# Kernel tuning notes

Hardware: AMD Instinct MI355X
Metric: run time of the kernel (lower is better)

The kernel has to match this reference:

```python
import jax, jax.numpy as jnp
import numpy as np

B, N, H, NB, NCT = 8, 4096, 1024, 128, 33
LN_EPS = 1e-5


def setup_inputs() -> dict:
    key = jax.random.key(0)
    ks = jax.random.split(key, 12)
    x = jax.random.normal(ks[0], (B, N, H), dtype=jnp.float32)
    cancer_type = jax.random.randint(ks[1], (B,), 0, NCT)
    block_ids = jax.random.randint(ks[2], (B, N), 0, NB)
    pad_mask = jnp.zeros((B, N), dtype=bool)
    s1 = 1.0 / np.sqrt(H)
    s2 = 1.0 / np.sqrt(H // 2)
    return {
        "x": x,
        "cancer_type": cancer_type,
        "block_ids": block_ids,
        "pad_mask": pad_mask,
        "W1": jax.random.normal(ks[3], (H, H // 2), jnp.float32) * s1,
        "b1": jnp.zeros((H // 2,), jnp.float32),
        "W2": jax.random.normal(ks[4], (H // 2, 1), jnp.float32) * s2,
        "b2": jnp.zeros((1,), jnp.float32),
        "ct_emb": jax.random.normal(ks[5], (NCT, NB), jnp.float32) * 0.1,
        "Wp": jax.random.normal(ks[6], (H, H), jnp.float32) * s1,
        "bp": jnp.zeros((H,), jnp.float32),
        "ln_g": jnp.ones((H,), jnp.float32),
        "ln_b": jnp.zeros((H,), jnp.float32),
    }


def reference(x, cancer_type, block_ids, pad_mask, W1, b1, W2, b2, ct_emb, Wp, bp, ln_g, ln_b):
    nb = ct_emb.shape[1]
    # gate MLP: (B,N)
    h = jnp.tanh(x @ W1 + b1)
    gate = (h @ W2 + b2)[..., 0]
    valid = ~pad_mask
    # block membership mask (B, NB, N)
    mask = (block_ids[:, None, :] == jnp.arange(nb)[None, :, None]) & valid[:, None, :]
    neg_inf = jnp.float32(-jnp.inf)
    scores = jnp.where(mask, gate[:, None, :], neg_inf)
    # stable masked softmax over N; empty blocks -> all-zero weights (nan_to_num(0))
    m = jnp.max(scores, axis=-1, keepdims=True)
    m = jnp.where(jnp.isfinite(m), m, 0.0)
    e = jnp.where(mask, jnp.exp(scores - m), 0.0)
    denom = jnp.sum(e, axis=-1, keepdims=True)
    w = jnp.where(denom > 0, e / jnp.maximum(denom, 1e-30), 0.0)
    # cancer-type modulation: weights * (1 + 0.1*ct_mod[:,bid])
    ct_mod = ct_emb[cancer_type]  # (B, NB)
    w = w * (1.0 + 0.1 * ct_mod)[:, :, None]
    # pooled per-block token (B, NB, H)
    pooled = jnp.einsum('bkn,bnh->bkh', w, x)
    # block_proj: Linear -> LayerNorm -> ELU (dropout = eval identity)
    y = pooled @ Wp + bp
    mu = jnp.mean(y, axis=-1, keepdims=True)
    var = jnp.mean((y - mu) ** 2, axis=-1, keepdims=True)
    y = (y - mu) * jax.lax.rsqrt(var + LN_EPS) * ln_g + ln_b
    y = jax.nn.elu(y)
    has_b = jnp.any(mask, axis=-1)              # (B, NB)
    present = jnp.any(has_b, axis=0)            # (NB,) torch loop skips blocks absent everywhere
    block_tokens = jnp.where(present[None, :, None], y, 0.0)
    return block_tokens, has_b
```

## Files before the change

kernel.cpp:

```cpp
#include <hip/hip_runtime.h>

#define NTOK 4096
#define HDIM 1024
#define HHALF 512
#define NBLK 128
#define CAP 256

typedef __attribute__((ext_vector_type(8))) short short8;
typedef __attribute__((ext_vector_type(4))) float f32x4;
typedef short bf16s;

__device__ __forceinline__ short f2bf(float f) {
    unsigned u = __builtin_bit_cast(unsigned, f);
    u = (u + 0x7fffu + ((u >> 16) & 1u)) >> 16;
    return (short)u;
}
__device__ __forceinline__ void gload_lds16(const void* g, void* l) {
    __builtin_amdgcn_global_load_lds(
        (const __attribute__((address_space(1))) unsigned int*)g,
        (__attribute__((address_space(3))) unsigned int*)l, 16, 0, 0);
}
__device__ __forceinline__ float fast_tanh(float v) {
    float e = __expf(2.0f * v);
    return 1.0f - 2.0f / (e + 1.0f);
}

__global__ void k_tcvt2(const float* __restrict__ W1, const float* __restrict__ Wp,
                        bf16s* __restrict__ w1t, bf16s* __restrict__ wpt) {
    __shared__ float tile[64][65];
    const int by = blockIdx.y;
    const float* in = (by < 8) ? W1 : Wp;
    bf16s* out = (by < 8) ? w1t : wpt;
    const int Nc = (by < 8) ? HHALF : HDIM;
    const int n0 = ((by < 8) ? by : (by - 8)) * 64;
    const int k0 = blockIdx.x * 64;
    const int tx = threadIdx.x & 63, ty = threadIdx.x >> 6;
    #pragma unroll
    for (int i = 0; i < 16; ++i) {
        int r = ty + i * 4;
        tile[r][tx] = in[(size_t)(k0 + r) * Nc + n0 + tx];
    }
    __syncthreads();
    #pragma unroll
    for (int i = 0; i < 16; ++i) {
        int r = ty + i * 4;
        out[(size_t)(n0 + r) * 1024 + k0 + tx] = f2bf(tile[tx][r]);
    }
}

__global__ __launch_bounds__(256, 3) void k_gemm_gf(
    const float* __restrict__ x, const bf16s* __restrict__ w1t,
    const float* __restrict__ b1, const float* __restrict__ w2,
    float* __restrict__ partial)
{
    __shared__ alignas(16) float As[2][128 * 32];
    __shared__ alignas(16) bf16s Bs[2][128 * 32];
    __shared__ float gp[2][128];

    const int tid = threadIdx.x;
    const int lane = tid & 63;
    const int wv = tid >> 6;
    const int wr = wv >> 1, wc = wv & 1;
    const int phys = blockIdx.x;
    const int logical = (phys & 7) * 128 + (phys >> 3);
    const int row0 = (logical >> 2) * 128;
    const int col0 = (logical & 3) * 128;
    const int c0 = lane & 15, khalf = lane >> 4;

    const int aRow = wv * 32 + (lane >> 3);
    const int aj = (lane & 7) ^ ((lane >> 3) & 7);
    const float* aSrc = &x[(size_t)(row0 + aRow) * HDIM + aj * 4];
    const int adst = wv * 1024 + lane * 4;

    const int bRow = wv * 32 + (lane >> 2);
    const int bj = (lane & 3) ^ ((lane >> 3) & 3);
    const bf16s* bSrc = &w1t[(size_t)(col0 + bRow) * HDIM + bj * 8];
    const int bdst = wv * 1024 + lane * 8;

    f32x4 acc[4][4] = {};

    #pragma unroll
    for (int q = 0; q < 4; ++q)
        gload_lds16(aSrc + q * 8 * HDIM, &As[0][adst + q * 256]);
    #pragma unroll
    for (int q = 0; q < 2; ++q)
        gload_lds16(bSrc + q * 16 * HDIM, &Bs[0][bdst + q * 512]);

    for (int t = 0; t < 32; ++t) {
        const int cur = t & 1;
        if (t < 31) {
            const int ko = (t + 1) * 32;
            #pragma unroll
            for (int q = 0; q < 4; ++q)
                gload_lds16(aSrc + q * 8 * HDIM + ko, &As[cur ^ 1][adst + q * 256]);
            #pragma unroll
            for (int q = 0; q < 2; ++q)
                gload_lds16(bSrc + q * 16 * HDIM + ko, &Bs[cur ^ 1][bdst + q * 512]);
            asm volatile("s_waitcnt vmcnt(6)" ::: "memory");
        } else {
            asm volatile("s_waitcnt vmcnt(0)" ::: "memory");
        }
        __builtin_amdgcn_s_barrier();
        __builtin_amdgcn_sched_barrier(0);

        short8 av[4], bv[4];
        #pragma unroll
        for (int mf = 0; mf < 4; ++mf) {
            int ra = wr * 64 + mf * 16 + c0;
            f32x4 lo = *reinterpret_cast<const f32x4*>(
                &As[cur][ra * 32 + (((2 * khalf) ^ (ra & 7)) * 4)]);
            f32x4 hi = *reinterpret_cast<const f32x4*>(
                &As[cur][ra * 32 + (((2 * khalf + 1) ^ (ra & 7)) * 4)]);
            short h[8] = {f2bf(lo[0]), f2bf(lo[1]), f2bf(lo[2]), f2bf(lo[3]),
                          f2bf(hi[0]), f2bf(hi[1]), f2bf(hi[2]), f2bf(hi[3])};
            av[mf] = *reinterpret_cast<const short8*>(h);
        }
        #pragma unroll
        for (int nf = 0; nf < 4; ++nf) {
            int rb = wc * 64 + nf * 16 + c0;
            bv[nf] = *reinterpret_cast<const short8*>(
                &Bs[cur][rb * 32 + ((khalf ^ ((rb >> 1) & 3)) * 8)]);
        }

        __builtin_amdgcn_s_setprio(1);
        #pragma unroll
        for (int nf = 0; nf < 4; ++nf)
            #pragma unroll
            for (int mf = 0; mf < 4; ++mf)
                acc[mf][nf] = __builtin_amdgcn_mfma_f32_16x16x32_bf16(av[mf], bv[nf], acc[mf][nf], 0, 0, 0);
        __builtin_amdgcn_s_setprio(0);

        asm volatile("s_waitcnt lgkmcnt(0)" ::: "memory");
        __builtin_amdgcn_sched_barrier(0);
        __builtin_amdgcn_s_barrier();
    }

    float b1v[4], w2v[4];
    #pragma unroll
    for (int nf = 0; nf < 4; ++nf) {
        int gc = col0 + wc * 64 + nf * 16 + c0;
        b1v[nf] = b1[gc];
        w2v[nf] = w2[gc];
    }
    #pragma unroll
    for (int mf = 0; mf < 4; ++mf) {
        #pragma unroll
        for (int reg = 0; reg < 4; ++reg) {
            float s = 0.f;
            #pragma unroll
            for (int nf = 0; nf < 4; ++nf)
                s += fast_tanh(acc[mf][nf][reg] + b1v[nf]) * w2v[nf];
            s += __shfl_xor(s, 1); s += __shfl_xor(s, 2);
            s += __shfl_xor(s, 4); s += __shfl_xor(s, 8);
            if (c0 == 0) gp[wc][wr * 64 + mf * 16 + khalf * 4 + reg] = s;
        }
    }
    __syncthreads();
    if (tid < 128)
        partial[(size_t)(logical & 3) * 32768 + row0 + tid] = gp[0][tid] + gp[1][tid];
}

__global__ void k_blocks(const int* __restrict__ block_ids, const unsigned char* __restrict__ pad,
                         const float* __restrict__ part, const float* __restrict__ b2,
                         float* __restrict__ gate, const int* __restrict__ ct,
                         const float* __restrict__ ct_emb,
                         int* __restrict__ counts, float* __restrict__ mblk,
                         float* __restrict__ wscale, int* __restrict__ lists,
                         float* __restrict__ out_hasb)
{
    const int blk = blockIdx.x;
    const int b = blk >> 7, k = blk & 127;
    const int lane = threadIdx.x;
    const int base = b * NTOK;
    const int lbase = blk * CAP;
    const unsigned long long ltmask = (1ull << lane) - 1ull;
    const float b2v = b2[0];

    float m = -__builtin_inff();
    float s = 0.f;
    int pos = 0;
    for (int t0 = 0; t0 < NTOK; t0 += 64) {
        int t = t0 + lane;
        bool mt = (block_ids[base + t] == k) && (pad[base + t] == 0);
        unsigned long long mask = __ballot(mt);
        if (mt) {
            int r = base + t;
            float g = part[r] + part[32768 + r] + part[65536 + r] + part[98304 + r] + b2v;
            gate[r] = g;
            int my = pos + __popcll(mask & ltmask);
            if (my < CAP) lists[lbase + my] = t;
            float mn = fmaxf(m, g);
            s = s * __expf(m - mn) + __expf(g - mn);
            m = mn;
        }
        pos += __popcll(mask);
    }
    #pragma unroll
    for (int off = 1; off < 64; off <<= 1) {
        float om = __shfl_xor(m, off);
        float os = __shfl_xor(s, off);
        float mn = fmaxf(m, om);
        float sa = (m == -__builtin_inff()) ? 0.f : s * __expf(m - mn);
        float sb = (om == -__builtin_inff()) ? 0.f : os * __expf(om - mn);
        s = sa + sb;
        m = mn;
    }
    if (lane == 0) {
        counts[blk] = pos;
        mblk[blk] = (pos > 0) ? m : 0.f;
        float mod = 1.0f + 0.1f * ct_emb[ct[b] * NBLK + k];
        wscale[blk] = (pos > 0 && s > 0.f) ? (mod / fmaxf(s, 1e-30f)) : 0.f;
        out_hasb[blk] = (pos > 0) ? 1.f : 0.f;
    }
}

__global__ void k_pool(const float* __restrict__ x, const float* __restrict__ gate,
                       const int* __restrict__ lists, const int* __restrict__ counts,
                       const float* __restrict__ mblk, const float* __restrict__ wscale,
                       bf16s* __restrict__ pooled)
{
    const int blk = blockIdx.x;
    const int b = blk >> 7;
    const int tid = threadIdx.x;
    const int base = b * NTOK;
    const int cnt = min(counts[blk], CAP);
    const int lbase = blk * CAP;
    const float m = mblk[blk], ws = wscale[blk];

    float4 acc = {0.f, 0.f, 0.f, 0.f};
    for (int i = 0; i < cnt; ++i) {
        int n = lists[lbase + i];
        float w = __expf(gate[base + n] - m);
        float4 xv = *reinterpret_cast<const float4*>(&x[(size_t)(base + n) * HDIM + tid * 4]);
        acc.x += w * xv.x; acc.y += w * xv.y; acc.z += w * xv.z; acc.w += w * xv.w;
    }
    short o[4] = {f2bf(acc.x * ws), f2bf(acc.y * ws), f2bf(acc.z * ws), f2bf(acc.w * ws)};
    *reinterpret_cast<int2*>(&pooled[(size_t)blk * HDIM + tid * 4]) =
        *reinterpret_cast<const int2*>(o);
}

__global__ __launch_bounds__(256) void k_gemm2(
    const bf16s* __restrict__ pooled, const bf16s* __restrict__ wpt,
    const float* __restrict__ bp, float* __restrict__ y)
{
    __shared__ alignas(16) bf16s As[2][64 * 32];
    __shared__ alignas(16) bf16s Bs[2][64 * 32];
    const int tid = threadIdx.x;
    const int lane = tid & 63;
    const int wv = tid >> 6;
    const int wr = wv >> 1, wc = wv & 1;
    const int row0 = (blockIdx.x >> 4) * 64, col0 = (blockIdx.x & 15) * 64;
    const int c0 = lane & 15, khalf = lane >> 4;

    const int sr = wv * 16 + (lane >> 2);
    const int sj = (lane & 3) ^ ((sr >> 1) & 3);
    const int sdst = (wv * 16) * 32 + lane * 8;
    const bf16s* srcA = &pooled[(size_t)(row0 + sr) * 1024 + sj * 8];
    const bf16s* srcB = &wpt[(size_t)(col0 + sr) * 1024 + sj * 8];

    f32x4 acc[2][2] = {};

    gload_lds16(srcA, &As[0][sdst]);
    gload_lds16(srcB, &Bs[0][sdst]);

    for (int t = 0; t < 32; ++t) {
        const int cur = t & 1;
        if (t < 31) {
            gload_lds16(srcA + (t + 1) * 32, &As[cur ^ 1][sdst]);
            gload_lds16(srcB + (t + 1) * 32, &Bs[cur ^ 1][sdst]);
            asm volatile("s_waitcnt vmcnt(2)" ::: "memory");
        } else {
            asm volatile("s_waitcnt vmcnt(0)" ::: "memory");
        }
        __builtin_amdgcn_s_barrier();
        __builtin_amdgcn_sched_barrier(0);
        #pragma unroll
        for (int mf = 0; mf < 2; ++mf) {
            int ra = wr * 32 + mf * 16 + c0;
            short8 av = *reinterpret_cast<const short8*>(
                &As[cur][ra * 32 + ((khalf ^ ((ra >> 1) & 3)) * 8)]);
            #pragma unroll
            for (int nf = 0; nf < 2; ++nf) {
                int rb = wc * 32 + nf * 16 + c0;
                short8 bv = *reinterpret_cast<const short8*>(
                    &Bs[cur][rb * 32 + ((khalf ^ ((rb >> 1) & 3)) * 8)]);
                acc[mf][nf] = __builtin_amdgcn_mfma_f32_16x16x32_bf16(av, bv, acc[mf][nf], 0, 0, 0);
            }
        }
        asm volatile("s_waitcnt lgkmcnt(0)" ::: "memory");
        __builtin_amdgcn_sched_barrier(0);
        __builtin_amdgcn_s_barrier();
    }
    #pragma unroll
    for (int mf = 0; mf < 2; ++mf)
        #pragma unroll
        for (int nf = 0; nf < 2; ++nf)
            #pragma unroll
            for (int reg = 0; reg < 4; ++reg) {
                int grow = row0 + wr * 32 + mf * 16 + khalf * 4 + reg;
                int gcol = col0 + wc * 32 + nf * 16 + c0;
                y[(size_t)grow * 1024 + gcol] = acc[mf][nf][reg] + bp[gcol];
            }
}

__global__ void k_lnelu(const float* __restrict__ y, const float* __restrict__ ln_g,
                        const float* __restrict__ ln_b, const int* __restrict__ counts,
                        float* __restrict__ outp)
{
    const int row = blockIdx.x;
    const int k = row & 127;
    const int tid = threadIdx.x;

    float4 v = *reinterpret_cast<const float4*>(&y[(size_t)row * 1024 + tid * 4]);
    float s = v.x + v.y + v.z + v.w;
    float ss = v.x * v.x + v.y * v.y + v.z * v.z + v.w * v.w;
    #pragma unroll
    for (int off = 32; off; off >>= 1) { s += __shfl_xor(s, off); ss += __shfl_xor(ss, off); }

    __shared__ float sbuf[4], ssbuf[4];
    int wv = tid >> 6;
    if ((tid & 63) == 0) { sbuf[wv] = s; ssbuf[wv] = ss; }
    __syncthreads();
    s = sbuf[0] + sbuf[1] + sbuf[2] + sbuf[3];
    ss = ssbuf[0] + ssbuf[1] + ssbuf[2] + ssbuf[3];

    float mu = s * (1.f / 1024.f);
    float var = ss * (1.f / 1024.f) - mu * mu;
    float rstd = rsqrtf(var + 1e-5f);

    bool pres = false;
    #pragma unroll
    for (int bb = 0; bb < 8; ++bb) pres = pres || (counts[bb * NBLK + k] > 0);

    float4 g4 = *reinterpret_cast<const float4*>(&ln_g[tid * 4]);
    float4 b4 = *reinterpret_cast<const float4*>(&ln_b[tid * 4]);
    float vals[4] = {v.x, v.y, v.z, v.w};
    float gs[4] = {g4.x, g4.y, g4.z, g4.w};
    float bs[4] = {b4.x, b4.y, b4.z, b4.w};
    float4 o;
    float* op = &o.x;
    #pragma unroll
    for (int j = 0; j < 4; ++j) {
        float t = (vals[j] - mu) * rstd * gs[j] + bs[j];
        t = (t > 0.f) ? t : expm1f(t);
        op[j] = pres ? t : 0.f;
    }
    *reinterpret_cast<float4*>(&outp[(size_t)row * 1024 + tid * 4]) = o;
}

extern "C" void kernel_launch(void* const* d_in, const int* in_sizes, int n_in,
                              void* d_out, int out_size, void* d_ws, size_t ws_size,
                              hipStream_t stream)
{
    const float* x      = (const float*)d_in[0];
    const int*   ct     = (const int*)d_in[1];
    const int*   bids   = (const int*)d_in[2];
    const unsigned char* pad = (const unsigned char*)d_in[3];
    const float* W1     = (const float*)d_in[4];
    const float* b1     = (const float*)d_in[5];
    const float* W2     = (const float*)d_in[6];
    const float* b2     = (const float*)d_in[7];
    const float* ct_emb = (const float*)d_in[8];
    const float* Wp     = (const float*)d_in[9];
    const float* bp     = (const float*)d_in[10];
    const float* ln_g   = (const float*)d_in[11];
    const float* ln_b   = (const float*)d_in[12];
    float* outF = (float*)d_out;

    char* ws = (char*)d_ws;
    bf16s* w1t    = (bf16s*)(ws + 0);
    bf16s* wpt    = (bf16s*)(ws + 1048576);
    float* gate   = (float*)(ws + 3145728);
    float* part   = (float*)(ws + 3276800);
    float* mblk   = (float*)(ws + 3801088);
    float* wscal  = (float*)(ws + 3805184);
    int*   counts = (int*)  (ws + 3809280);
    int*   lists  = (int*)  (ws + 3813376);
    bf16s* pooled = (bf16s*)(ws + 4861952);
    float* ybuf   = (float*)(ws + 6959104);

    k_tcvt2<<<dim3(16, 24), 256, 0, stream>>>(W1, Wp, w1t, wpt);
    k_gemm_gf<<<1024, 256, 0, stream>>>(x, w1t, b1, W2, part);
    k_blocks<<<1024, 64, 0, stream>>>(bids, pad, part, b2, gate, ct, ct_emb,
                                      counts, mblk, wscal, lists,
                                      outF + (size_t)8 * NBLK * HDIM);
    k_pool<<<1024, 256, 0, stream>>>(x, gate, lists, counts, mblk, wscal, pooled);
    k_gemm2<<<256, 256, 0, stream>>>(pooled, wpt, bp, ybuf);
    k_lnelu<<<1024, 256, 0, stream>>>(ybuf, ln_g, ln_b, counts, outF);
}
```

Before: 151.8 us.

## Pre-convert x to bf16 once and triple-buffer the gate GEMM

Adds a streaming kernel that converts x to bf16 in the workspace. The gate GEMM then loads bf16 tiles for both operands with a shared swizzle, and the per-tile fp32 to bf16 conversion in its inner loop is gone. The k-loop moves from double to triple buffering with deeper vmcnt waits, and the pooling kernel reads the bf16 copy of x. In exchange it adds one extra full pass over x (fp32 read plus bf16 write), and pooling now accumulates from rounded bf16 inputs, which lowers its precision.

```diff
diff --git a/kernel.cpp b/kernel.cpp
--- a/kernel.cpp
+++ b/kernel.cpp
@@ -5,6 +5,7 @@
 #define HHALF 512
 #define NBLK 128
 #define CAP 256
+#define XELEMS 33554432ull
 
 typedef __attribute__((ext_vector_type(8))) short short8;
 typedef __attribute__((ext_vector_type(4))) float f32x4;
@@ -23,6 +24,17 @@
 __device__ __forceinline__ float fast_tanh(float v) {
     float e = __expf(2.0f * v);
     return 1.0f - 2.0f / (e + 1.0f);
+}
+
+__global__ void k_xcvt(const float* __restrict__ in, bf16s* __restrict__ out) {
+    for (size_t i = ((size_t)blockIdx.x * 256 + threadIdx.x) * 8; i < XELEMS;
+         i += (size_t)gridDim.x * 256 * 8) {
+        float4 a = *reinterpret_cast<const float4*>(&in[i]);
+        float4 b = *reinterpret_cast<const float4*>(&in[i + 4]);
+        short h[8] = {f2bf(a.x), f2bf(a.y), f2bf(a.z), f2bf(a.w),
+                      f2bf(b.x), f2bf(b.y), f2bf(b.z), f2bf(b.w)};
+        *reinterpret_cast<int4*>(&out[i]) = *reinterpret_cast<const int4*>(h);
+    }
 }
 
 __global__ void k_tcvt2(const float* __restrict__ W1, const float* __restrict__ Wp,
@@ -48,14 +60,13 @@
     }
 }
 
-__global__ __launch_bounds__(256, 3) void k_gemm_gf(
-    const float* __restrict__ x, const bf16s* __restrict__ w1t,
+__global__ __launch_bounds__(256, 3) void k_gemm_g(
+    const bf16s* __restrict__ xb, const bf16s* __restrict__ w1t,
     const float* __restrict__ b1, const float* __restrict__ w2,
     float* __restrict__ partial)
 {
-    __shared__ alignas(16) float As[2][128 * 32];
-    __shared__ alignas(16) bf16s Bs[2][128 * 32];
-    __shared__ float gp[2][128];
+    __shared__ alignas(16) bf16s As[3][128 * 32];
+    __shared__ alignas(16) bf16s Bs[3][128 * 32];
 
     const int tid = threadIdx.x;
     const int lane = tid & 63;
@@ -67,36 +78,38 @@
     const int col0 = (logical & 3) * 128;
     const int c0 = lane & 15, khalf = lane >> 4;
 
-    const int aRow = wv * 32 + (lane >> 3);
-    const int aj = (lane & 7) ^ ((lane >> 3) & 7);
-    const float* aSrc = &x[(size_t)(row0 + aRow) * HDIM + aj * 4];
-    const int adst = wv * 1024 + lane * 4;
-
-    const int bRow = wv * 32 + (lane >> 2);
-    const int bj = (lane & 3) ^ ((lane >> 3) & 3);
-    const bf16s* bSrc = &w1t[(size_t)(col0 + bRow) * HDIM + bj * 8];
-    const int bdst = wv * 1024 + lane * 8;
+    const int srow = wv * 32 + (lane >> 2);
+    const int sj = (lane & 3) ^ ((srow >> 1) & 3);
+    const bf16s* aSrc = &xb [(size_t)(row0 + srow) * HDIM + sj * 8];
+    const bf16s* bSrc = &w1t[(size_t)(col0 + srow) * HDIM + sj * 8];
+    const int sdst = (wv * 32) * 32 + lane * 8;
 
     f32x4 acc[4][4] = {};
 
     #pragma unroll
-    for (int q = 0; q < 4; ++q)
-        gload_lds16(aSrc + q * 8 * HDIM, &As[0][adst + q * 256]);
-    #pragma unroll
-    for (int q = 0; q < 2; ++q)
-        gload_lds16(bSrc + q * 16 * HDIM, &Bs[0][bdst + q * 512]);
+    for (int q = 0; q < 2; ++q) {
+        gload_lds16(aSrc + q * 16 * HDIM, &As[0][sdst + q * 512]);
+        gload_lds16(bSrc + q * 16 * HDIM, &Bs[0][sdst + q * 512]);
+    }
+    #pragma unroll
+    for (int q = 0; q < 2; ++q) {
+        gload_lds16(aSrc + q * 16 * HDIM + 32, &As[1][sdst + q * 512]);
+        gload_lds16(bSrc + q * 16 * HDIM + 32, &Bs[1][sdst + q * 512]);
+    }
 
     for (int t = 0; t < 32; ++t) {
-        const int cur = t & 1;
-        if (t < 31) {
-            const int ko = (t + 1) * 32;
+        const int cur = t % 3;
+        if (t < 30) {
+            const int nb = (t + 2) % 3;
+            const int ko = (t + 2) * 32;
             #pragma unroll
-            for (int q = 0; q < 4; ++q)
-                gload_lds16(aSrc + q * 8 * HDIM + ko, &As[cur ^ 1][adst + q * 256]);
-            #pragma unroll
-            for (int q = 0; q < 2; ++q)
-                gload_lds16(bSrc + q * 16 * HDIM + ko, &Bs[cur ^ 1][bdst + q * 512]);
-            asm volatile("s_waitcnt vmcnt(6)" ::: "memory");
+            for (int q = 0; q < 2; ++q) {
+                gload_lds16(aSrc + q * 16 * HDIM + ko, &As[nb][sdst + q * 512]);
+                gload_lds16(bSrc + q * 16 * HDIM + ko, &Bs[nb][sdst + q * 512]);
+            }
+            asm volatile("s_waitcnt vmcnt(8)" ::: "memory");
+        } else if (t == 30) {
+            asm volatile("s_waitcnt vmcnt(4)" ::: "memory");
         } else {
             asm volatile("s_waitcnt vmcnt(0)" ::: "memory");
         }
@@ -107,13 +120,8 @@
         #pragma unroll
         for (int mf = 0; mf < 4; ++mf) {
             int ra = wr * 64 + mf * 16 + c0;
-            f32x4 lo = *reinterpret_cast<const f32x4*>(
-                &As[cur][ra * 32 + (((2 * khalf) ^ (ra & 7)) * 4)]);
-            f32x4 hi = *reinterpret_cast<const f32x4*>(
-                &As[cur][ra * 32 + (((2 * khalf + 1) ^ (ra & 7)) * 4)]);
-            short h[8] = {f2bf(lo[0]), f2bf(lo[1]), f2bf(lo[2]), f2bf(lo[3]),
-                          f2bf(hi[0]), f2bf(hi[1]), f2bf(hi[2]), f2bf(hi[3])};
-            av[mf] = *reinterpret_cast<const short8*>(h);
+            av[mf] = *reinterpret_cast<const short8*>(
+                &As[cur][ra * 32 + ((khalf ^ ((ra >> 1) & 3)) * 8)]);
         }
         #pragma unroll
         for (int nf = 0; nf < 4; ++nf) {
@@ -135,6 +143,7 @@
         __builtin_amdgcn_s_barrier();
     }
 
+    float* gp = reinterpret_cast<float*>(&As[0][0]);
     float b1v[4], w2v[4];
     #pragma unroll
     for (int nf = 0; nf < 4; ++nf) {
@@ -152,12 +161,12 @@
                 s += fast_tanh(acc[mf][nf][reg] + b1v[nf]) * w2v[nf];
             s += __shfl_xor(s, 1); s += __shfl_xor(s, 2);
             s += __shfl_xor(s, 4); s += __shfl_xor(s, 8);
-            if (c0 == 0) gp[wc][wr * 64 + mf * 16 + khalf * 4 + reg] = s;
+            if (c0 == 0) gp[wc * 128 + wr * 64 + mf * 16 + khalf * 4 + reg] = s;
         }
     }
     __syncthreads();
     if (tid < 128)
-        partial[(size_t)(logical & 3) * 32768 + row0 + tid] = gp[0][tid] + gp[1][tid];
+        partial[(size_t)(logical & 3) * 32768 + row0 + tid] = gp[tid] + gp[128 + tid];
 }
 
 __global__ void k_blocks(const int* __restrict__ block_ids, const unsigned char* __restrict__ pad,
@@ -214,7 +223,7 @@
     }
 }
 
-__global__ void k_pool(const float* __restrict__ x, const float* __restrict__ gate,
+__global__ void k_pool(const bf16s* __restrict__ xb, const float* __restrict__ gate,
                        const int* __restrict__ lists, const int* __restrict__ counts,
                        const float* __restrict__ mblk, const float* __restrict__ wscale,
                        bf16s* __restrict__ pooled)
@@ -231,8 +240,17 @@
     for (int i = 0; i < cnt; ++i) {
         int n = lists[lbase + i];
         float w = __expf(gate[base + n] - m);
-        float4 xv = *reinterpret_cast<const float4*>(&x[(size_t)(base + n) * HDIM + tid * 4]);
-        acc.x += w * xv.x; acc.y += w * xv.y; acc.z += w * xv.z; acc.w += w * xv.w;
+        int2 rv = *reinterpret_cast<const int2*>(&xb[(size_t)(base + n) * HDIM + tid * 4]);
+        short s4[4];
+        *reinterpret_cast<int2*>(s4) = rv;
+        unsigned u0 = ((unsigned)(unsigned short)s4[0]) << 16;
+        unsigned u1 = ((unsigned)(unsigned short)s4[1]) << 16;
+        unsigned u2 = ((unsigned)(unsigned short)s4[2]) << 16;
+        unsigned u3 = ((unsigned)(unsigned short)s4[3]) << 16;
+        acc.x += w * __builtin_bit_cast(float, u0);
+        acc.y += w * __builtin_bit_cast(float, u1);
+        acc.z += w * __builtin_bit_cast(float, u2);
+        acc.w += w * __builtin_bit_cast(float, u3);
     }
     short o[4] = {f2bf(acc.x * ws), f2bf(acc.y * ws), f2bf(acc.z * ws), f2bf(acc.w * ws)};
     *reinterpret_cast<int2*>(&pooled[(size_t)blk * HDIM + tid * 4]) =
@@ -378,13 +396,15 @@
     int*   lists  = (int*)  (ws + 3813376);
     bf16s* pooled = (bf16s*)(ws + 4861952);
     float* ybuf   = (float*)(ws + 6959104);
+    bf16s* xb     = (bf16s*)(ws + 11153408);
 
     k_tcvt2<<<dim3(16, 24), 256, 0, stream>>>(W1, Wp, w1t, wpt);
-    k_gemm_gf<<<1024, 256, 0, stream>>>(x, w1t, b1, W2, part);
+    k_xcvt<<<2048, 256, 0, stream>>>(x, xb);
+    k_gemm_g<<<1024, 256, 0, stream>>>(xb, w1t, b1, W2, part);
     k_blocks<<<1024, 64, 0, stream>>>(bids, pad, part, b2, gate, ct, ct_emb,
                                       counts, mblk, wscal, lists,
                                       outF + (size_t)8 * NBLK * HDIM);
-    k_pool<<<1024, 256, 0, stream>>>(x, gate, lists, counts, mblk, wscal, pooled);
+    k_pool<<<1024, 256, 0, stream>>>(xb, gate, lists, counts, mblk, wscal, pooled);
     k_gemm2<<<256, 256, 0, stream>>>(pooled, wpt, bp, ybuf);
     k_lnelu<<<1024, 256, 0, stream>>>(ybuf, ln_g, ln_b, counts, outF);
 }
```

After: 159.1 us. 1.05x slower.

## Widen gate GEMM tile to 128x256 and convert x to bf16 before LDS

Applied to the files above, without the earlier changes.

The gate GEMM now uses 128x256 output tiles, so each workgroup covers half of the 512 hidden columns and x is read twice instead of four times. Each wave now owns a 128x64 slice. x is loaded through registers, converted to bf16 once, and stored in a swizzled LDS layout, so waves no longer repeat the fp32-to-bf16 conversion on every LDS read. This also halves the A-tile LDS footprint. The cost is double the accumulator registers (occupancy bound drops from 3 to 2), register-staged A loads in place of direct global-to-LDS copies, and fewer workgroups (512). The k_blocks kernel now sums two partial gate buffers instead of four.

```diff
diff --git a/kernel.cpp b/kernel.cpp
--- a/kernel.cpp
+++ b/kernel.cpp
@@ -48,102 +48,122 @@
     }
 }
 
-__global__ __launch_bounds__(256, 3) void k_gemm_gf(
+__global__ __launch_bounds__(256, 2) void k_gemmv(
     const float* __restrict__ x, const bf16s* __restrict__ w1t,
     const float* __restrict__ b1, const float* __restrict__ w2,
     float* __restrict__ partial)
 {
-    __shared__ alignas(16) float As[2][128 * 32];
-    __shared__ alignas(16) bf16s Bs[2][128 * 32];
-    __shared__ float gp[2][128];
+    __shared__ alignas(16) bf16s As[2][128 * 32];
+    __shared__ alignas(16) bf16s Bs[2][256 * 32];
 
     const int tid = threadIdx.x;
     const int lane = tid & 63;
-    const int wv = tid >> 6;
-    const int wr = wv >> 1, wc = wv & 1;
+    const int wn = tid >> 6;
     const int phys = blockIdx.x;
-    const int logical = (phys & 7) * 128 + (phys >> 3);
-    const int row0 = (logical >> 2) * 128;
-    const int col0 = (logical & 3) * 128;
+    const int logical = (phys & 7) * 64 + (phys >> 3);
+    const int rp = logical >> 1;
+    const int ctile = logical & 1;
+    const int row0 = rp * 128;
+    const int col0 = ctile * 256;
     const int c0 = lane & 15, khalf = lane >> 4;
 
-    const int aRow = wv * 32 + (lane >> 3);
-    const int aj = (lane & 7) ^ ((lane >> 3) & 7);
-    const float* aSrc = &x[(size_t)(row0 + aRow) * HDIM + aj * 4];
-    const int adst = wv * 1024 + lane * 4;
-
-    const int bRow = wv * 32 + (lane >> 2);
-    const int bj = (lane & 3) ^ ((lane >> 3) & 3);
-    const bf16s* bSrc = &w1t[(size_t)(col0 + bRow) * HDIM + bj * 8];
-    const int bdst = wv * 1024 + lane * 8;
-
-    f32x4 acc[4][4] = {};
-
+    const int ar = tid >> 1, ah = tid & 1;
+    const float* aF = &x[(size_t)(row0 + ar) * HDIM + ah * 16];
+    const int akey = (ar >> 1) & 3;
+    const int aslot0 = ((2 * ah) ^ akey) * 8;
+    const int aslot1 = ((2 * ah + 1) ^ akey) * 8;
+    const int arow32 = ar * 32;
+
+    const int sj = (lane & 3) ^ ((lane >> 3) & 3);
+    const bf16s* bS[4];
+    int bdst[4];
+    #pragma unroll
+    for (int q = 0; q < 4; ++q) {
+        int rb = wn * 64 + q * 16 + (lane >> 2);
+        bS[q] = &w1t[(size_t)(col0 + rb) * HDIM + sj * 8];
+        bdst[q] = (wn * 64 + q * 16) * 32 + lane * 8;
+    }
+
+    const int fkey = (c0 >> 1) & 3;
+    const int ach = (khalf ^ fkey) * 8;
+    const int arA = c0 * 32 + ach;
+    const int brB = (wn * 64 + c0) * 32 + ach;
+
+    f32x4 acc[8][4] = {};
+    float4 rA0, rA1, rA2, rA3;
+
+#define LOAD_RA(T) do {                                               \
+        rA0 = *reinterpret_cast<const float4*>(aF + (T) * 32);        \
+        rA1 = *reinterpret_cast<const float4*>(aF + (T) * 32 + 4);    \
+        rA2 = *reinterpret_cast<const float4*>(aF + (T) * 32 + 8);    \
+        rA3 = *reinterpret_cast<const float4*>(aF + (T) * 32 + 12);   \
+    } while (0)
+#define CVTWR(BUF) do {                                               \
+        short h_[16] = {f2bf(rA0.x), f2bf(rA0.y), f2bf(rA0.z), f2bf(rA0.w), \
+                        f2bf(rA1.x), f2bf(rA1.y), f2bf(rA1.z), f2bf(rA1.w), \
+                        f2bf(rA2.x), f2bf(rA2.y), f2bf(rA2.z), f2bf(rA2.w), \
+                        f2bf(rA3.x), f2bf(rA3.y), f2bf(rA3.z), f2bf(rA3.w)};\
+        *reinterpret_cast<int4*>(&As[BUF][arow32 + aslot0]) =         \
+            *reinterpret_cast<const int4*>(&h_[0]);                   \
+        *reinterpret_cast<int4*>(&As[BUF][arow32 + aslot1]) =         \
+            *reinterpret_cast<const int4*>(&h_[8]);                   \
+    } while (0)
+
+    LOAD_RA(0);
+    CVTWR(0);
     #pragma unroll
     for (int q = 0; q < 4; ++q)
-        gload_lds16(aSrc + q * 8 * HDIM, &As[0][adst + q * 256]);
-    #pragma unroll
-    for (int q = 0; q < 2; ++q)
-        gload_lds16(bSrc + q * 16 * HDIM, &Bs[0][bdst + q * 512]);
+        gload_lds16(bS[q], &Bs[0][bdst[q]]);
+    LOAD_RA(1);
 
     for (int t = 0; t < 32; ++t) {
-        const int cur = t & 1;
+        const int c = t & 1;
         if (t < 31) {
-            const int ko = (t + 1) * 32;
             #pragma unroll
             for (int q = 0; q < 4; ++q)
-                gload_lds16(aSrc + q * 8 * HDIM + ko, &As[cur ^ 1][adst + q * 256]);
-            #pragma unroll
-            for (int q = 0; q < 2; ++q)
-                gload_lds16(bSrc + q * 16 * HDIM + ko, &Bs[cur ^ 1][bdst + q * 512]);
-            asm volatile("s_waitcnt vmcnt(6)" ::: "memory");
+                gload_lds16(bS[q] + (t + 1) * 32, &Bs[c ^ 1][bdst[q]]);
+            __builtin_amdgcn_sched_barrier(0);
+            CVTWR(c ^ 1);
+            if (t < 30) LOAD_RA(t + 2);
         } else {
             asm volatile("s_waitcnt vmcnt(0)" ::: "memory");
         }
-        __builtin_amdgcn_s_barrier();
-        __builtin_amdgcn_sched_barrier(0);
-
-        short8 av[4], bv[4];
-        #pragma unroll
-        for (int mf = 0; mf < 4; ++mf) {
-            int ra = wr * 64 + mf * 16 + c0;
-            f32x4 lo = *reinterpret_cast<const f32x4*>(
-                &As[cur][ra * 32 + (((2 * khalf) ^ (ra & 7)) * 4)]);
-            f32x4 hi = *reinterpret_cast<const f32x4*>(
-                &As[cur][ra * 32 + (((2 * khalf + 1) ^ (ra & 7)) * 4)]);
-            short h[8] = {f2bf(lo[0]), f2bf(lo[1]), f2bf(lo[2]), f2bf(lo[3]),
-                          f2bf(hi[0]), f2bf(hi[1]), f2bf(hi[2]), f2bf(hi[3])};
-            av[mf] = *reinterpret_cast<const short8*>(h);
-        }
-        #pragma unroll
-        for (int nf = 0; nf < 4; ++nf) {
-            int rb = wc * 64 + nf * 16 + c0;
-            bv[nf] = *reinterpret_cast<const short8*>(
-                &Bs[cur][rb * 32 + ((khalf ^ ((rb >> 1) & 3)) * 8)]);
-        }
-
-        __builtin_amdgcn_s_setprio(1);
-        #pragma unroll
-        for (int nf = 0; nf < 4; ++nf)
-            #pragma unroll
-            for (int mf = 0; mf < 4; ++mf)
-                acc[mf][nf] = __builtin_amdgcn_mfma_f32_16x16x32_bf16(av[mf], bv[nf], acc[mf][nf], 0, 0, 0);
-        __builtin_amdgcn_s_setprio(0);
-
         asm volatile("s_waitcnt lgkmcnt(0)" ::: "memory");
         __builtin_amdgcn_sched_barrier(0);
         __builtin_amdgcn_s_barrier();
-    }
-
+
+        short8 av[8], bvv[4];
+        #pragma unroll
+        for (int mf = 0; mf < 8; ++mf)
+            av[mf] = *reinterpret_cast<const short8*>(&As[c][arA + mf * 512]);
+        #pragma unroll
+        for (int nf = 0; nf < 4; ++nf)
+            bvv[nf] = *reinterpret_cast<const short8*>(&Bs[c][brB + nf * 512]);
+        asm volatile("s_waitcnt lgkmcnt(0)" ::: "memory");
+        __builtin_amdgcn_sched_barrier(0);
+
+        __builtin_amdgcn_s_setprio(1);
+        #pragma unroll
+        for (int nf = 0; nf < 4; ++nf)
+            #pragma unroll
+            for (int mf = 0; mf < 8; ++mf)
+                acc[mf][nf] = __builtin_amdgcn_mfma_f32_16x16x32_bf16(av[mf], bvv[nf], acc[mf][nf], 0, 0, 0);
+        __builtin_amdgcn_s_setprio(0);
+    }
+#undef LOAD_RA
+#undef CVTWR
+
+    __syncthreads();
+    float* gp = reinterpret_cast<float*>(&As[0][0]);
     float b1v[4], w2v[4];
     #pragma unroll
     for (int nf = 0; nf < 4; ++nf) {
-        int gc = col0 + wc * 64 + nf * 16 + c0;
+        int gc = col0 + wn * 64 + nf * 16 + c0;
         b1v[nf] = b1[gc];
         w2v[nf] = w2[gc];
     }
     #pragma unroll
-    for (int mf = 0; mf < 4; ++mf) {
+    for (int mf = 0; mf < 8; ++mf) {
         #pragma unroll
         for (int reg = 0; reg < 4; ++reg) {
             float s = 0.f;
@@ -152,12 +172,13 @@
                 s += fast_tanh(acc[mf][nf][reg] + b1v[nf]) * w2v[nf];
             s += __shfl_xor(s, 1); s += __shfl_xor(s, 2);
             s += __shfl_xor(s, 4); s += __shfl_xor(s, 8);
-            if (c0 == 0) gp[wc][wr * 64 + mf * 16 + khalf * 4 + reg] = s;
+            if (c0 == 0) gp[wn * 128 + mf * 16 + khalf * 4 + reg] = s;
         }
     }
     __syncthreads();
     if (tid < 128)
-        partial[(size_t)(logical & 3) * 32768 + row0 + tid] = gp[0][tid] + gp[1][tid];
+        partial[(size_t)ctile * 32768 + row0 + tid] =
+            gp[tid] + gp[128 + tid] + gp[256 + tid] + gp[384 + tid];
 }
 
 __global__ void k_blocks(const int* __restrict__ block_ids, const unsigned char* __restrict__ pad,
@@ -185,7 +206,7 @@
         unsigned long long mask = __ballot(mt);
         if (mt) {
             int r = base + t;
-            float g = part[r] + part[32768 + r] + part[65536 + r] + part[98304 + r] + b2v;
+            float g = part[r] + part[32768 + r] + b2v;
             gate[r] = g;
             int my = pos + __popcll(mask & ltmask);
             if (my < CAP) lists[lbase + my] = t;
@@ -380,7 +401,7 @@
     float* ybuf   = (float*)(ws + 6959104);
 
     k_tcvt2<<<dim3(16, 24), 256, 0, stream>>>(W1, Wp, w1t, wpt);
-    k_gemm_gf<<<1024, 256, 0, stream>>>(x, w1t, b1, W2, part);
+    k_gemmv<<<512, 256, 0, stream>>>(x, w1t, b1, W2, part);
     k_blocks<<<1024, 64, 0, stream>>>(bids, pad, part, b2, gate, ct, ct_emb,
                                       counts, mblk, wscal, lists,
                                       outF + (size_t)8 * NBLK * HDIM);
```

Result: faster. 125.9 us (median of 2 runs) (-17.1%).
